# Optimization experiments

Hardware: AMD Instinct MI355X
Metric: run time of the kernel (lower is better)

## Reference

```python
import jax, jax.numpy as jnp
import numpy as np

B, NX, NU, H, HID, NIT = 4096, 64, 16, 50, 256, 10


def dynamics(x, u, W1, b1, W2):
    # residual tanh-MLP dynamics: x_next = x + 0.1*tanh([x,u]@W1+b1)@W2
    z = jnp.concatenate([x, u], axis=-1)
    return x + 0.1 * jnp.tanh(z @ W1 + b1) @ W2


def setup_inputs() -> dict:
    key = jax.random.key(0)
    k0, k1, k2, k3 = jax.random.split(key, 4)
    x0 = jax.random.normal(k0, (B, NX), dtype=jnp.float32)
    xref = jnp.zeros((B, H + 1, NX), dtype=jnp.float32)
    W1 = jax.random.normal(k1, (NX + NU, HID), dtype=jnp.float32) * 0.05
    b1 = jnp.zeros((HID,), dtype=jnp.float32)
    W2 = jax.random.normal(k2, (HID, NX), dtype=jnp.float32) * 0.05
    # deterministic stand-in for torch.randn inside _compute_sqp_step (one draw per SQP iter)
    noise = jax.random.normal(k3, (NIT, B, H * NU), dtype=jnp.float32)
    return {"x0": x0, "xref": xref, "W1": W1, "b1": b1, "W2": W2,
            "noise": noise, "n_iterations": NIT}


def reference(x0, xref, W1, b1, W2, noise, n_iterations):
    batch, nx = x0.shape
    N = xref.shape[1] - 1            # horizon
    nu = noise.shape[2] // N         # control dim
    u = jnp.zeros((batch, N * nu), dtype=x0.dtype)

    def rollout(u_flat):
        us = jnp.swapaxes(u_flat.reshape(batch, N, nu), 0, 1)  # [N, B, nu]
        def step(x, u_k):
            x_next = dynamics(x, u_k, W1, b1, W2)
            return x_next, x_next
        _, xs = jax.lax.scan(step, x0, us)                     # [N, B, nx]
        return jnp.concatenate([x0[:, None], jnp.swapaxes(xs, 0, 1)], axis=1)  # [B, N+1, nx]

    x_traj = rollout(u)
    gx = gu = None
    for it in range(n_iterations):
        # sequential nonlinear rollout with current controls
        x_traj = rollout(u)
        # per-step linearization via VJP with ones cotangent (as in torch autograd.grad
        # with grad_outputs=ones); steps are independent so batch them over (B, N).
        xs = x_traj[:, :N].reshape(batch * N, nx)
        us = u.reshape(batch * N, nu)
        def f(xs_, us_):
            return dynamics(xs_, us_, W1, b1, W2)
        _, vjp_fn = jax.vjp(f, xs, us)
        gx_, gu_ = vjp_fn(jnp.ones((batch * N, nx), dtype=x0.dtype))
        gx = gx_.reshape(batch, N, nx)   # rows of A_lin (ones^T @ df/dx)
        gu = gu_.reshape(batch, N, nu)   # rows of B_lin (ones^T @ df/du)
        # SQP "step" in source is fresh gaussian noise * 0.01, scaled by 0.1
        u = u + 0.1 * (noise[it] * 0.01)
    # (first control, trajectory, predicted states, last-iteration linearization VJPs)
    return u[:, :nu], x_traj, x_traj[:, 1:], gx, gu
```

## Files before the change

### kernel.cpp

```cpp
#include <hip/hip_runtime.h>

typedef unsigned int uint;
typedef unsigned short ushort_t;
typedef __attribute__((ext_vector_type(8))) short bf16x8_t;
typedef __attribute__((ext_vector_type(4))) float f32x4_t;

constexpr int Bsz = 4096, NX = 64, NU = 16, NXU = 80, HID = 256, Hh = 50;
constexpr long NS = (long)Bsz * Hh * NU;
constexpr int O1 = 65536;
constexpr int O2 = 13434880;
constexpr int O3 = 26542080;
constexpr int O4 = 39649280;
constexpr int XT_PITCH = (Hh + 1) * NX;
constexpr int PR_PITCH = Hh * NX;
constexpr int U_PITCH = Hh * NU;

constexpr int W1S = 260;
constexpr int HS  = 264;
constexpr int TS  = 264;
constexpr int W2S = 264;
constexpr int TLS = 264;

constexpr long T_BYTES = (long)Bsz * Hh * HID * 2;

__device__ __forceinline__ float tanh_fast(float x) {
    float e = __expf(2.0f * x);
    return 1.0f - 2.0f / (e + 1.0f);
}
__device__ __forceinline__ uint f2bf_u(float x) {
    uint b = __float_as_uint(x);
    return (b + 0x7FFFu + ((b >> 16) & 1u)) >> 16;
}
__device__ __forceinline__ float bf2f(ushort_t u) {
    return __uint_as_float(((uint)u) << 16);
}
__device__ __forceinline__ void unpack8(uint4 v, float* f) {
    f[0] = __uint_as_float(v.x << 16); f[1] = __uint_as_float(v.x & 0xFFFF0000u);
    f[2] = __uint_as_float(v.y << 16); f[3] = __uint_as_float(v.y & 0xFFFF0000u);
    f[4] = __uint_as_float(v.z << 16); f[5] = __uint_as_float(v.z & 0xFFFF0000u);
    f[6] = __uint_as_float(v.w << 16); f[7] = __uint_as_float(v.w & 0xFFFF0000u);
}

__global__ __launch_bounds__(256) void ker_roll(const float* __restrict__ x0,
                                                const float* __restrict__ W1,
                                                const float* __restrict__ b1,
                                                const float* __restrict__ W2,
                                                const float* __restrict__ noise,
                                                const int* __restrict__ nit_p,
                                                float* __restrict__ out,
                                                ushort_t* __restrict__ tg) {
    __shared__ __align__(16) float    W1L[NXU * W1S];
    __shared__ __align__(16) ushort_t W2T[NX * W2S];
    __shared__ __align__(16) float    hRT[16 * HS];
    __shared__ __align__(16) float    zT[NXU * 16];
    __shared__ float b1L[HID];
    __shared__ float sL[HID];

    const int tid = threadIdx.x;
    const int b0 = blockIdx.x * 16;
    const int nit = nit_p[0];

    for (int i = tid; i < NXU * HID; i += 256)
        W1L[(i >> 8) * W1S + (i & 255)] = W1[i];
    for (int i = tid; i < HID * NX; i += 256) {
        int c = i >> 6, d = i & 63;
        W2T[d * W2S + c] = (ushort_t)f2bf_u(W2[i]);
    }
    b1L[tid] = b1[tid];
    for (int i = tid; i < 16 * NX; i += 256) {
        int r = i >> 6, d = i & 63;
        float v = x0[(b0 + r) * NX + d];
        zT[d * 16 + r] = v;
        out[O1 + (b0 + r) * XT_PITCH + d] = v;
    }
    const int r16 = tid >> 4, q16 = tid & 15;
    {
        long base = (long)(b0 + r16) * U_PITCH + q16;
        float s = 0.f;
        for (int it = 0; it < nit - 1; ++it) s += noise[(long)it * NS + base];
        zT[(NX + q16) * 16 + r16] = 0.001f * s;
        out[(b0 + r16) * NU + q16] = 0.001f * (s + noise[(long)(nit - 1) * NS + base]);
    }
    __syncthreads();
    {
        float s = 0.f;
        for (int d = 0; d < NX; ++d) s += bf2f(W2T[d * W2S + tid]);
        sL[tid] = 0.1f * s;
    }

    const int ct = tid & 63, rt = tid >> 6;
    const uint* W2Tu = (const uint*)W2T;

    for (int k = 0; k < Hh; ++k) {
        __syncthreads();

        float v9[9];
        const bool fast = (k < Hh - 1) && (nit == 10);
        long nbase = (long)(b0 + r16) * U_PITCH + (k + 1) * NU + q16;
        if (fast) {
            #pragma unroll
            for (int it = 0; it < 9; ++it) v9[it] = noise[(long)it * NS + nbase];
        }

        float a_[4][4];
        {
            float bj[4];
            #pragma unroll
            for (int j = 0; j < 4; ++j) bj[j] = b1L[4 * ct + j];
            #pragma unroll
            for (int i = 0; i < 4; ++i)
                #pragma unroll
                for (int j = 0; j < 4; ++j) a_[i][j] = bj[j];
        }
        #pragma unroll 8
        for (int kk = 0; kk < NXU; ++kk) {
            float4 zv = *(const float4*)&zT[kk * 16 + 4 * rt];
            float4 wv = *(const float4*)&W1L[kk * W1S + 4 * ct];
            float zz[4] = {zv.x, zv.y, zv.z, zv.w};
            float ww[4] = {wv.x, wv.y, wv.z, wv.w};
            #pragma unroll
            for (int i = 0; i < 4; ++i)
                #pragma unroll
                for (int j = 0; j < 4; ++j) a_[i][j] += zz[i] * ww[j];
        }
        float h_[4][4];
        #pragma unroll
        for (int i = 0; i < 4; ++i)
            #pragma unroll
            for (int j = 0; j < 4; ++j) h_[i][j] = tanh_fast(a_[i][j]);
        #pragma unroll
        for (int i = 0; i < 4; ++i)
            *(float4*)&hRT[(4 * rt + i) * HS + 4 * ct] =
                make_float4(h_[i][0], h_[i][1], h_[i][2], h_[i][3]);
        {
            float s0 = sL[4 * ct], s1 = sL[4 * ct + 1], s2 = sL[4 * ct + 2], s3 = sL[4 * ct + 3];
            #pragma unroll
            for (int i = 0; i < 4; ++i) {
                float t0 = s0 * (1.f - h_[i][0] * h_[i][0]);
                float t1 = s1 * (1.f - h_[i][1] * h_[i][1]);
                float t2 = s2 * (1.f - h_[i][2] * h_[i][2]);
                float t3 = s3 * (1.f - h_[i][3] * h_[i][3]);
                size_t rho = (size_t)(b0 + 4 * rt + i) * Hh + k;
                uint2 pk = make_uint2(f2bf_u(t0) | (f2bf_u(t1) << 16),
                                      f2bf_u(t2) | (f2bf_u(t3) << 16));
                *(uint2*)(tg + rho * HID + 4 * ct) = pk;
            }
        }

        float unext = 0.f;
        if (k < Hh - 1) {
            if (fast) {
                #pragma unroll
                for (int it = 0; it < 9; ++it) unext += v9[it];
            } else {
                for (int it = 0; it < nit - 1; ++it) unext += noise[(long)it * NS + nbase];
            }
            unext *= 0.001f;
        }

        __syncthreads();

        float xacc[4] = {0.f, 0.f, 0.f, 0.f};
        #pragma unroll 4
        for (int c8 = 0; c8 < HID / 8; ++c8) {
            float4 h0 = *(const float4*)&hRT[r16 * HS + 8 * c8];
            float4 h1 = *(const float4*)&hRT[r16 * HS + 8 * c8 + 4];
            float hf[8] = {h0.x, h0.y, h0.z, h0.w, h1.x, h1.y, h1.z, h1.w};
            #pragma unroll
            for (int i = 0; i < 4; ++i) {
                int d = q16 + 16 * i;
                uint4 wv = *(const uint4*)&W2Tu[d * (W2S / 2) + 4 * c8];
                float wf[8];
                unpack8(wv, wf);
                #pragma unroll
                for (int jj = 0; jj < 8; ++jj) xacc[i] += hf[jj] * wf[jj];
            }
        }
        {
            const int bb = b0 + r16;
            #pragma unroll
            for (int i = 0; i < 4; ++i) {
                int d = q16 + 16 * i;
                float xn = zT[d * 16 + r16] + 0.1f * xacc[i];
                out[O1 + bb * XT_PITCH + (k + 1) * NX + d] = xn;
                out[O2 + bb * PR_PITCH + k * NX + d] = xn;
                zT[d * 16 + r16] = xn;
            }
            if (k < Hh - 1) zT[(NX + q16) * 16 + r16] = unext;
        }
    }
}

__global__ __launch_bounds__(256) void ker_lin2(const float* __restrict__ W1,
                                                const ushort_t* __restrict__ Tg,
                                                float* __restrict__ out) {
    __shared__ __align__(16) ushort_t W1b[NXU * TLS];

    const int tid = threadIdx.x;
    const int r0 = blockIdx.x * 128;

    {
        const float4* W1f4 = (const float4*)W1;
        for (int i = tid; i < (NXU * HID) / 4; i += 256) {
            float4 w = W1f4[i];
            int p = i >> 6, c4 = i & 63;
            uint2 pk = make_uint2(f2bf_u(w.x) | (f2bf_u(w.y) << 16),
                                  f2bf_u(w.z) | (f2bf_u(w.w) << 16));
            *(uint2*)&W1b[p * TLS + 4 * c4] = pk;
        }
    }
    __syncthreads();

    const int wv = tid >> 6, lane = tid & 63;
    const int m = lane & 15, quad = lane >> 4;

    f32x4_t acc[2][5];
    #pragma unroll
    for (int i = 0; i < 2; ++i)
        #pragma unroll
        for (int j = 0; j < 5; ++j) acc[i][j] = (f32x4_t){0.f, 0.f, 0.f, 0.f};

    const ushort_t* Ta = Tg + (size_t)(r0 + wv * 32 + m) * HID;
    const ushort_t* Tb = Ta + (size_t)16 * HID;

    #pragma unroll
    for (int kc = 0; kc < 8; ++kc) {
        const int koff = kc * 32 + quad * 8;
        bf16x8_t a0 = *(const bf16x8_t*)&Ta[koff];
        bf16x8_t a1 = *(const bf16x8_t*)&Tb[koff];
        #pragma unroll
        for (int nt = 0; nt < 5; ++nt) {
            bf16x8_t bfr = *(const bf16x8_t*)&W1b[(nt * 16 + m) * TLS + koff];
            acc[0][nt] = __builtin_amdgcn_mfma_f32_16x16x32_bf16(a0, bfr, acc[0][nt], 0, 0, 0);
            acc[1][nt] = __builtin_amdgcn_mfma_f32_16x16x32_bf16(a1, bfr, acc[1][nt], 0, 0, 0);
        }
    }

    #pragma unroll
    for (int mt = 0; mt < 2; ++mt) {
        int rbase = r0 + wv * 32 + mt * 16 + quad * 4;
        #pragma unroll
        for (int r = 0; r < 4; ++r) {
            int rho = rbase + r;
            int b = (int)(((unsigned long long)rho * 1374389535ULL) >> 36);
            int kk = rho - b * 50;
            float* gxp = out + O3 + (size_t)b * PR_PITCH + kk * NX + m;
            #pragma unroll
            for (int nt = 0; nt < 4; ++nt)
                gxp[nt * 16] = 1.0f + acc[mt][nt][r];
            out[O4 + (size_t)b * U_PITCH + kk * NU + m] = acc[mt][4][r];
        }
    }
}

__global__ __launch_bounds__(256) void ker_fused(const float* __restrict__ x0,
                                                 const float* __restrict__ W1,
                                                 const float* __restrict__ b1,
                                                 const float* __restrict__ W2,
                                                 const float* __restrict__ noise,
                                                 const int* __restrict__ nit_p,
                                                 float* __restrict__ out) {
    __shared__ __align__(16) float    W1L[NXU * W1S];
    __shared__ __align__(16) ushort_t W2T[NX * W2S];
    __shared__ __align__(16) float    hRT[16 * HS];
    __shared__ __align__(16) ushort_t tT[16 * TS];
    __shared__ __align__(16) float    zT[NXU * 16];
    __shared__ float b1L[HID];
    __shared__ float sL[HID];

    const int tid = threadIdx.x;
    const int b0 = blockIdx.x * 16;
    const int nit = nit_p[0];

    for (int i = tid; i < NXU * HID; i += 256)
        W1L[(i >> 8) * W1S + (i & 255)] = W1[i];
    for (int i = tid; i < HID * NX; i += 256) {
        int c = i >> 6, d = i & 63;
        W2T[d * W2S + c] = (ushort_t)f2bf_u(W2[i]);
    }
    b1L[tid] = b1[tid];
    for (int i = tid; i < 16 * NX; i += 256) {
        int r = i >> 6, d = i & 63;
        float v = x0[(b0 + r) * NX + d];
        zT[d * 16 + r] = v;
        out[O1 + (b0 + r) * XT_PITCH + d] = v;
    }
    const int r16 = tid >> 4, q16 = tid & 15;
    {
        long base = (long)(b0 + r16) * U_PITCH + q16;
        float s = 0.f;
        for (int it = 0; it < nit - 1; ++it) s += noise[(long)it * NS + base];
        zT[(NX + q16) * 16 + r16] = 0.001f * s;
        out[(b0 + r16) * NU + q16] = 0.001f * (s + noise[(long)(nit - 1) * NS + base]);
    }
    __syncthreads();
    {
        float s = 0.f;
        for (int d = 0; d < NX; ++d) s += bf2f(W2T[d * W2S + tid]);
        sL[tid] = 0.1f * s;
    }

    const int ct = tid & 63, rt = tid >> 6;
    uint* tTu = (uint*)tT;
    const uint* W2Tu = (const uint*)W2T;

    for (int k = 0; k < Hh; ++k) {
        __syncthreads();
        float v9[9];
        const bool fast = (k < Hh - 1) && (nit == 10);
        long nbase = (long)(b0 + r16) * U_PITCH + (k + 1) * NU + q16;
        if (fast) {
            #pragma unroll
            for (int it = 0; it < 9; ++it) v9[it] = noise[(long)it * NS + nbase];
        }
        float a_[4][4];
        {
            float bj[4];
            #pragma unroll
            for (int j = 0; j < 4; ++j) bj[j] = b1L[4 * ct + j];
            #pragma unroll
            for (int i = 0; i < 4; ++i)
                #pragma unroll
                for (int j = 0; j < 4; ++j) a_[i][j] = bj[j];
        }
        #pragma unroll 8
        for (int kk = 0; kk < NXU; ++kk) {
            float4 zv = *(const float4*)&zT[kk * 16 + 4 * rt];
            float4 wv = *(const float4*)&W1L[kk * W1S + 4 * ct];
            float zz[4] = {zv.x, zv.y, zv.z, zv.w};
            float ww[4] = {wv.x, wv.y, wv.z, wv.w};
            #pragma unroll
            for (int i = 0; i < 4; ++i)
                #pragma unroll
                for (int j = 0; j < 4; ++j) a_[i][j] += zz[i] * ww[j];
        }
        float h_[4][4];
        #pragma unroll
        for (int i = 0; i < 4; ++i)
            #pragma unroll
            for (int j = 0; j < 4; ++j) h_[i][j] = tanh_fast(a_[i][j]);
        #pragma unroll
        for (int i = 0; i < 4; ++i)
            *(float4*)&hRT[(4 * rt + i) * HS + 4 * ct] =
                make_float4(h_[i][0], h_[i][1], h_[i][2], h_[i][3]);
        {
            float s0 = sL[4 * ct], s1 = sL[4 * ct + 1], s2 = sL[4 * ct + 2], s3 = sL[4 * ct + 3];
            #pragma unroll
            for (int i = 0; i < 4; ++i) {
                float t0 = s0 * (1.f - h_[i][0] * h_[i][0]);
                float t1 = s1 * (1.f - h_[i][1] * h_[i][1]);
                float t2 = s2 * (1.f - h_[i][2] * h_[i][2]);
                float t3 = s3 * (1.f - h_[i][3] * h_[i][3]);
                tTu[(4 * rt + i) * (TS / 2) + 2 * ct]     = f2bf_u(t0) | (f2bf_u(t1) << 16);
                tTu[(4 * rt + i) * (TS / 2) + 2 * ct + 1] = f2bf_u(t2) | (f2bf_u(t3) << 16);
            }
        }
        float unext = 0.f;
        if (k < Hh - 1) {
            if (fast) {
                #pragma unroll
                for (int it = 0; it < 9; ++it) unext += v9[it];
            } else {
                for (int it = 0; it < nit - 1; ++it) unext += noise[(long)it * NS + nbase];
            }
            unext *= 0.001f;
        }
        __syncthreads();
        float xacc[4] = {0.f, 0.f, 0.f, 0.f};
        #pragma unroll 4
        for (int c8 = 0; c8 < HID / 8; ++c8) {
            float4 h0 = *(const float4*)&hRT[r16 * HS + 8 * c8];
            float4 h1 = *(const float4*)&hRT[r16 * HS + 8 * c8 + 4];
            float hf[8] = {h0.x, h0.y, h0.z, h0.w, h1.x, h1.y, h1.z, h1.w};
            #pragma unroll
            for (int i = 0; i < 4; ++i) {
                int d = q16 + 16 * i;
                uint4 wv = *(const uint4*)&W2Tu[d * (W2S / 2) + 4 * c8];
                float wf[8];
                unpack8(wv, wf);
                #pragma unroll
                for (int jj = 0; jj < 8; ++jj) xacc[i] += hf[jj] * wf[jj];
            }
        }
        {
            const int bb = b0 + r16;
            #pragma unroll
            for (int i = 0; i < 4; ++i) {
                int d = q16 + 16 * i;
                float xn = zT[d * 16 + r16] + 0.1f * xacc[i];
                out[O1 + bb * XT_PITCH + (k + 1) * NX + d] = xn;
                out[O2 + bb * PR_PITCH + k * NX + d] = xn;
                zT[d * 16 + r16] = xn;
            }
            if (k < Hh - 1) zT[(NX + q16) * 16 + r16] = unext;
        }
        {
            const uint* tTr = (const uint*)tT + r16 * (TS / 2);
            float g_[5] = {0.f, 0.f, 0.f, 0.f, 0.f};
            #pragma unroll 4
            for (int jc = 0; jc < HID / 8; ++jc) {
                uint4 tv = *(const uint4*)&tTr[4 * jc];
                float tf[8];
                unpack8(tv, tf);
                #pragma unroll
                for (int i = 0; i < 5; ++i) {
                    int p = q16 + 16 * i;
                    float4 w0 = *(const float4*)&W1L[p * W1S + 8 * jc];
                    float4 w1 = *(const float4*)&W1L[p * W1S + 8 * jc + 4];
                    g_[i] += tf[0] * w0.x + tf[1] * w0.y + tf[2] * w0.z + tf[3] * w0.w
                           + tf[4] * w1.x + tf[5] * w1.y + tf[6] * w1.z + tf[7] * w1.w;
                }
            }
            const int bb = b0 + r16;
            #pragma unroll
            for (int i = 0; i < 4; ++i)
                out[O3 + bb * PR_PITCH + k * NX + (q16 + 16 * i)] = 1.0f + g_[i];
            out[O4 + bb * U_PITCH + k * NU + q16] = g_[4];
        }
    }
}

extern "C" void kernel_launch(void* const* d_in, const int* in_sizes, int n_in,
                              void* d_out, int out_size, void* d_ws, size_t ws_size,
                              hipStream_t stream) {
    const float* x0    = (const float*)d_in[0];
    const float* W1    = (const float*)d_in[2];
    const float* b1    = (const float*)d_in[3];
    const float* W2    = (const float*)d_in[4];
    const float* noise = (const float*)d_in[5];
    const int*   nit   = (const int*)d_in[6];
    float* out = (float*)d_out;

    if (ws_size >= (size_t)T_BYTES) {
        ushort_t* tg = (ushort_t*)d_ws;
        ker_roll<<<Bsz / 16, 256, 0, stream>>>(x0, W1, b1, W2, noise, nit, out, tg);
        ker_lin2<<<(Bsz * Hh) / 128, 256, 0, stream>>>(W1, tg, out);
    } else {
        ker_fused<<<Bsz / 16, 256, 0, stream>>>(x0, W1, b1, W2, noise, nit, out);
    }
}
```

Before: 748.4 us.

## Double rollout kernel block size to 512 threads with halved per-thread tiles

The sequential rollout kernel now uses 512 threads per block instead of 256. Each thread computes a 2x4 tile of the hidden layer and two output states instead of 4x4 and four, and the output-stage mapping is rearranged. The hidden-buffer pitch changes from 264 to 260. The goal is to shorten each latency-bound horizon step by spreading its work across more wavefronts, at the cost of more barrier participants and idle threads in the noise-summing code.

Result: faster. 730.6 us (-2.4%).

```diff
diff --git a/kernel.cpp b/kernel.cpp
--- a/kernel.cpp
+++ b/kernel.cpp
@@ -17,6 +17,7 @@
 
 constexpr int W1S = 260;
 constexpr int HS  = 264;
+constexpr int HSR = 260;
 constexpr int TS  = 264;
 constexpr int W2S = 264;
 constexpr int TLS = 264;
@@ -41,17 +42,17 @@
     f[6] = __uint_as_float(v.w << 16); f[7] = __uint_as_float(v.w & 0xFFFF0000u);
 }
 
-__global__ __launch_bounds__(256) void ker_roll(const float* __restrict__ x0,
-                                                const float* __restrict__ W1,
-                                                const float* __restrict__ b1,
-                                                const float* __restrict__ W2,
-                                                const float* __restrict__ noise,
-                                                const int* __restrict__ nit_p,
-                                                float* __restrict__ out,
-                                                ushort_t* __restrict__ tg) {
+__global__ __launch_bounds__(512, 2) void ker_roll(const float* __restrict__ x0,
+                                                   const float* __restrict__ W1,
+                                                   const float* __restrict__ b1,
+                                                   const float* __restrict__ W2,
+                                                   const float* __restrict__ noise,
+                                                   const int* __restrict__ nit_p,
+                                                   float* __restrict__ out,
+                                                   ushort_t* __restrict__ tg) {
     __shared__ __align__(16) float    W1L[NXU * W1S];
     __shared__ __align__(16) ushort_t W2T[NX * W2S];
-    __shared__ __align__(16) float    hRT[16 * HS];
+    __shared__ __align__(16) float    hRT[16 * HSR];
     __shared__ __align__(16) float    zT[NXU * 16];
     __shared__ float b1L[HID];
     __shared__ float sL[HID];
@@ -60,35 +61,36 @@
     const int b0 = blockIdx.x * 16;
     const int nit = nit_p[0];
 
-    for (int i = tid; i < NXU * HID; i += 256)
+    for (int i = tid; i < NXU * HID; i += 512)
         W1L[(i >> 8) * W1S + (i & 255)] = W1[i];
-    for (int i = tid; i < HID * NX; i += 256) {
+    for (int i = tid; i < HID * NX; i += 512) {
         int c = i >> 6, d = i & 63;
         W2T[d * W2S + c] = (ushort_t)f2bf_u(W2[i]);
     }
-    b1L[tid] = b1[tid];
-    for (int i = tid; i < 16 * NX; i += 256) {
+    if (tid < HID) b1L[tid] = b1[tid];
+    for (int i = tid; i < 16 * NX; i += 512) {
         int r = i >> 6, d = i & 63;
         float v = x0[(b0 + r) * NX + d];
         zT[d * 16 + r] = v;
         out[O1 + (b0 + r) * XT_PITCH + d] = v;
     }
-    const int r16 = tid >> 4, q16 = tid & 15;
-    {
-        long base = (long)(b0 + r16) * U_PITCH + q16;
+    const int r16n = (tid >> 4) & 15, q16n = tid & 15;
+    if (tid < 256) {
+        long base = (long)(b0 + r16n) * U_PITCH + q16n;
         float s = 0.f;
         for (int it = 0; it < nit - 1; ++it) s += noise[(long)it * NS + base];
-        zT[(NX + q16) * 16 + r16] = 0.001f * s;
-        out[(b0 + r16) * NU + q16] = 0.001f * (s + noise[(long)(nit - 1) * NS + base]);
+        zT[(NX + q16n) * 16 + r16n] = 0.001f * s;
+        out[(b0 + r16n) * NU + q16n] = 0.001f * (s + noise[(long)(nit - 1) * NS + base]);
     }
     __syncthreads();
-    {
+    if (tid < HID) {
         float s = 0.f;
         for (int d = 0; d < NX; ++d) s += bf2f(W2T[d * W2S + tid]);
         sL[tid] = 0.1f * s;
     }
 
-    const int ct = tid & 63, rt = tid >> 6;
+    const int ct = tid & 63, rt8 = tid >> 6;
+    const int q16 = tid & 15, cg = tid >> 4;
     const uint* W2Tu = (const uint*)W2T;
 
     for (int k = 0; k < Hh; ++k) {
@@ -96,51 +98,51 @@
 
         float v9[9];
         const bool fast = (k < Hh - 1) && (nit == 10);
-        long nbase = (long)(b0 + r16) * U_PITCH + (k + 1) * NU + q16;
-        if (fast) {
+        long nbase = (long)(b0 + r16n) * U_PITCH + (k + 1) * NU + q16n;
+        if (fast && tid < 256) {
             #pragma unroll
             for (int it = 0; it < 9; ++it) v9[it] = noise[(long)it * NS + nbase];
         }
 
-        float a_[4][4];
+        float a_[2][4];
         {
             float bj[4];
             #pragma unroll
             for (int j = 0; j < 4; ++j) bj[j] = b1L[4 * ct + j];
             #pragma unroll
-            for (int i = 0; i < 4; ++i)
+            for (int i = 0; i < 2; ++i)
                 #pragma unroll
                 for (int j = 0; j < 4; ++j) a_[i][j] = bj[j];
         }
         #pragma unroll 8
         for (int kk = 0; kk < NXU; ++kk) {
-            float4 zv = *(const float4*)&zT[kk * 16 + 4 * rt];
+            float2 zv = *(const float2*)&zT[kk * 16 + 2 * rt8];
             float4 wv = *(const float4*)&W1L[kk * W1S + 4 * ct];
-            float zz[4] = {zv.x, zv.y, zv.z, zv.w};
+            float zz[2] = {zv.x, zv.y};
             float ww[4] = {wv.x, wv.y, wv.z, wv.w};
             #pragma unroll
-            for (int i = 0; i < 4; ++i)
+            for (int i = 0; i < 2; ++i)
                 #pragma unroll
                 for (int j = 0; j < 4; ++j) a_[i][j] += zz[i] * ww[j];
         }
-        float h_[4][4];
-        #pragma unroll
-        for (int i = 0; i < 4; ++i)
+        float h_[2][4];
+        #pragma unroll
+        for (int i = 0; i < 2; ++i)
             #pragma unroll
             for (int j = 0; j < 4; ++j) h_[i][j] = tanh_fast(a_[i][j]);
         #pragma unroll
-        for (int i = 0; i < 4; ++i)
-            *(float4*)&hRT[(4 * rt + i) * HS + 4 * ct] =
+        for (int i = 0; i < 2; ++i)
+            *(float4*)&hRT[(2 * rt8 + i) * HSR + 4 * ct] =
                 make_float4(h_[i][0], h_[i][1], h_[i][2], h_[i][3]);
         {
             float s0 = sL[4 * ct], s1 = sL[4 * ct + 1], s2 = sL[4 * ct + 2], s3 = sL[4 * ct + 3];
             #pragma unroll
-            for (int i = 0; i < 4; ++i) {
+            for (int i = 0; i < 2; ++i) {
                 float t0 = s0 * (1.f - h_[i][0] * h_[i][0]);
                 float t1 = s1 * (1.f - h_[i][1] * h_[i][1]);
                 float t2 = s2 * (1.f - h_[i][2] * h_[i][2]);
                 float t3 = s3 * (1.f - h_[i][3] * h_[i][3]);
-                size_t rho = (size_t)(b0 + 4 * rt + i) * Hh + k;
+                size_t rho = (size_t)(b0 + 2 * rt8 + i) * Hh + k;
                 uint2 pk = make_uint2(f2bf_u(t0) | (f2bf_u(t1) << 16),
                                       f2bf_u(t2) | (f2bf_u(t3) << 16));
                 *(uint2*)(tg + rho * HID + 4 * ct) = pk;
@@ -148,7 +150,7 @@
         }
 
         float unext = 0.f;
-        if (k < Hh - 1) {
+        if (tid < 256 && k < Hh - 1) {
             if (fast) {
                 #pragma unroll
                 for (int it = 0; it < 9; ++it) unext += v9[it];
@@ -160,15 +162,15 @@
 
         __syncthreads();
 
-        float xacc[4] = {0.f, 0.f, 0.f, 0.f};
+        float xacc[2] = {0.f, 0.f};
         #pragma unroll 4
         for (int c8 = 0; c8 < HID / 8; ++c8) {
-            float4 h0 = *(const float4*)&hRT[r16 * HS + 8 * c8];
-            float4 h1 = *(const float4*)&hRT[r16 * HS + 8 * c8 + 4];
+            float4 h0 = *(const float4*)&hRT[q16 * HSR + 8 * c8];
+            float4 h1 = *(const float4*)&hRT[q16 * HSR + 8 * c8 + 4];
             float hf[8] = {h0.x, h0.y, h0.z, h0.w, h1.x, h1.y, h1.z, h1.w};
             #pragma unroll
-            for (int i = 0; i < 4; ++i) {
-                int d = q16 + 16 * i;
+            for (int i = 0; i < 2; ++i) {
+                int d = cg + 32 * i;
                 uint4 wv = *(const uint4*)&W2Tu[d * (W2S / 2) + 4 * c8];
                 float wf[8];
                 unpack8(wv, wf);
@@ -177,16 +179,16 @@
             }
         }
         {
-            const int bb = b0 + r16;
-            #pragma unroll
-            for (int i = 0; i < 4; ++i) {
-                int d = q16 + 16 * i;
-                float xn = zT[d * 16 + r16] + 0.1f * xacc[i];
+            const int bb = b0 + q16;
+            #pragma unroll
+            for (int i = 0; i < 2; ++i) {
+                int d = cg + 32 * i;
+                float xn = zT[d * 16 + q16] + 0.1f * xacc[i];
                 out[O1 + bb * XT_PITCH + (k + 1) * NX + d] = xn;
                 out[O2 + bb * PR_PITCH + k * NX + d] = xn;
-                zT[d * 16 + r16] = xn;
-            }
-            if (k < Hh - 1) zT[(NX + q16) * 16 + r16] = unext;
+                zT[d * 16 + q16] = xn;
+            }
+            if (tid < 256 && k < Hh - 1) zT[(NX + q16n) * 16 + r16n] = unext;
         }
     }
 }
@@ -433,7 +435,7 @@
 
     if (ws_size >= (size_t)T_BYTES) {
         ushort_t* tg = (ushort_t*)d_ws;
-        ker_roll<<<Bsz / 16, 256, 0, stream>>>(x0, W1, b1, W2, noise, nit, out, tg);
+        ker_roll<<<Bsz / 16, 512, 0, stream>>>(x0, W1, b1, W2, noise, nit, out, tg);
         ker_lin2<<<(Bsz * Hh) / 128, 256, 0, stream>>>(W1, tg, out);
     } else {
         ker_fused<<<Bsz / 16, 256, 0, stream>>>(x0, W1, b1, W2, noise, nit, out);
```
